# Optimization experiments

Hardware: AMD Instinct MI355X
Metric: run time of the kernel (lower is better)

## Reference

```python
import jax, jax.numpy as jnp
import numpy as np

WS = 8   # window_size
SS = 4   # shift_size
NH = 6   # num_heads
EPS = 1e-5


def _win_partition(x, ws):
    # x: [B, H, W, C] -> [B * H/ws * W/ws, ws*ws, C]
    B, H, W, C = x.shape
    x = x.reshape(B, H // ws, ws, W // ws, ws, C)
    return x.transpose(0, 1, 3, 2, 4, 5).reshape(-1, ws * ws, C)


def _win_reverse(wins, ws, H, W, B):
    C = wins.shape[-1]
    x = wins.reshape(B, H // ws, W // ws, ws, ws, C)
    return x.transpose(0, 1, 3, 2, 4, 5).reshape(B, H, W, C)


def _rel_pos_index(ws):
    # static numpy computation, identical to the torch buffer
    coords = np.stack(np.meshgrid(np.arange(ws), np.arange(ws), indexing='ij')).reshape(2, -1)
    rel = coords[:, :, None] - coords[:, None, :]          # [2, N, N]
    rel = rel.transpose(1, 2, 0).copy()                    # [N, N, 2]
    rel[..., 0] += ws - 1
    rel[..., 1] += ws - 1
    rel[..., 0] *= 2 * ws - 1
    return rel.sum(-1)                                     # [N, N] int


def _attn_mask_np(H, W, ws, ss):
    # static numpy computation of the SW-MSA mask, identical to _compute_mask
    img = np.zeros((1, H, W, 1), np.float32)
    cnt = 0
    for hs in (slice(0, -ws), slice(-ws, -ss), slice(-ss, None)):
        for wsl in (slice(0, -ws), slice(-ws, -ss), slice(-ss, None)):
            img[:, hs, wsl, :] = cnt
            cnt += 1
    mw = img.reshape(1, H // ws, ws, W // ws, ws, 1).transpose(0, 1, 3, 2, 4, 5).reshape(-1, ws * ws)
    am = mw[:, None, :] - mw[:, :, None]                   # [nW, N, N]
    return np.where(am != 0, np.float32(-100.0), np.float32(0.0))


def _swin_forward(x, qkv_w, qkv_b, proj_w, proj_b, rpb_table,
                  norm2_g, norm2_b, mlp_w1, mlp_b1, mlp_w2, mlp_b2, H, W):
    B, L, C = x.shape
    ws, ss, nh = WS, SS, NH
    hd = C // nh
    x2d = x.reshape(B, H, W, C)
    shifted = jnp.roll(x2d, (-ss, -ss), axis=(1, 2))
    win = _win_partition(shifted, ws)                      # [B_, N, C]
    B_, N, _ = win.shape

    # --- window attention (note: original applies attention to un-normalized x) ---
    qkv = (win @ qkv_w + qkv_b).reshape(B_, N, 3, nh, hd)
    q = qkv[:, :, 0].transpose(0, 2, 1, 3)                 # [B_, nh, N, hd]
    k = qkv[:, :, 1].transpose(0, 2, 1, 3)
    v = qkv[:, :, 2].transpose(0, 2, 1, 3)
    attn = jnp.einsum('bhnd,bhmd->bhnm', q, k) * (hd ** -0.5)

    bias = rpb_table[jnp.asarray(_rel_pos_index(ws)).reshape(-1)]
    bias = bias.reshape(N, N, nh).transpose(2, 0, 1)       # [nh, N, N]
    attn = attn + bias[None]

    mask = jnp.asarray(_attn_mask_np(H, W, ws, ss))        # [nW, N, N]
    nW = mask.shape[0]
    attn = attn.reshape(B_ // nW, nW, nh, N, N) + mask[None, :, None]
    attn = jax.nn.softmax(attn.reshape(B_, nh, N, N), axis=-1)

    out = jnp.einsum('bhnm,bhmd->bnhd', attn, v).reshape(B_, N, C)
    out = out @ proj_w + proj_b

    x2d = _win_reverse(out, ws, H, W, B)
    x2d = jnp.roll(x2d, (ss, ss), axis=(1, 2))
    x = x + x2d.reshape(B, L, C)

    # --- MLP branch with LayerNorm (norm2) ---
    mu = x.mean(-1, keepdims=True)
    var = x.var(-1, keepdims=True)
    xn = (x - mu) * jax.lax.rsqrt(var + EPS) * norm2_g + norm2_b
    h = jax.nn.gelu(xn @ mlp_w1 + mlp_b1, approximate=False)
    return x + (h @ mlp_w2 + mlp_b2)


def setup_inputs() -> dict:
    B, H, W, C = 8, 128, 128, 192
    mlp_hidden = 4 * C
    ks = jax.random.split(jax.random.key(0), 6)
    std = 0.02
    return {
        'x': jax.random.normal(ks[0], (B, H * W, C), jnp.float32),
        'qkv_w': jax.random.normal(ks[1], (C, 3 * C), jnp.float32) * std,
        'qkv_b': jnp.zeros((3 * C,), jnp.float32),
        'proj_w': jax.random.normal(ks[2], (C, C), jnp.float32) * std,
        'proj_b': jnp.zeros((C,), jnp.float32),
        'rpb_table': jax.random.normal(ks[3], ((2 * WS - 1) ** 2, NH), jnp.float32) * std,
        'norm2_g': jnp.ones((C,), jnp.float32),
        'norm2_b': jnp.zeros((C,), jnp.float32),
        'mlp_w1': jax.random.normal(ks[4], (C, mlp_hidden), jnp.float32) * std,
        'mlp_b1': jnp.zeros((mlp_hidden,), jnp.float32),
        'mlp_w2': jax.random.normal(ks[5], (mlp_hidden, C), jnp.float32) * std,
        'mlp_b2': jnp.zeros((C,), jnp.float32),
        'H': H,
        'W': W,
    }


def reference(x, qkv_w, qkv_b, proj_w, proj_b, rpb_table, norm2_g, norm2_b,
              mlp_w1, mlp_b1, mlp_w2, mlp_b2, H, W):
    return _swin_forward(x, qkv_w, qkv_b, proj_w, proj_b, rpb_table,
                         norm2_g, norm2_b, mlp_w1, mlp_b1, mlp_w2, mlp_b2, H, W)
```

## Files before the change

kernel.cpp:

```cpp
#include <hip/hip_runtime.h>
#include <hip/hip_bf16.h>


typedef __hip_bfloat16 bf16;
typedef __attribute__((ext_vector_type(8))) short bfrag;
typedef __attribute__((ext_vector_type(4))) float ffrag;

union bfu { bf16 h[8]; bfrag v; };

__device__ __forceinline__ float b2f(bf16 v) { return __bfloat162float(v); }
__device__ __forceinline__ bf16  f2b(float v) { return __float2bfloat16(v); }

#define MFMA(a, b, c) __builtin_amdgcn_mfma_f32_16x16x32_bf16((a), (b), (c), 0, 0, 0)

#define WS_XRES  0ULL
#define WS_OG    100663296ULL
#define WS_QKVTG 150994944ULL
#define WS_QBG   151250944ULL
#define WS_PROJT 151253504ULL
#define WS_W1T   151330304ULL
#define WS_W2T   151637504ULL
#define WS_SB    151969280ULL

__device__ __forceinline__ void stage_lds(const void* g, void* l, int nbytes, int t) {
    const int lane16 = (t & 63) * 16;
    for (int base = (t >> 6) * 1024; base < nbytes; base += 4096) {
        if (base + lane16 < nbytes) {
            __builtin_amdgcn_global_load_lds(
                (const __attribute__((address_space(1))) void*)((const char*)g + base + lane16),
                (__attribute__((address_space(3))) void*)((char*)l + base),
                16, 0, 0);
        }
    }
}

__device__ __forceinline__ float gelu_t(float x) {
    float y = x * (1.5957691216057308f + 0.07135481627f * x * x);
    return x * (1.f / (1.f + __expf(-y)));
}

__global__ __launch_bounds__(256) void k_prep(
    const float* __restrict__ qkv_w, const float* __restrict__ qkv_b,
    const float* __restrict__ proj_w, const float* __restrict__ w1,
    const float* __restrict__ w2, const float* __restrict__ rpb,
    char* __restrict__ ws)
{
    int i = blockIdx.x * 256 + threadIdx.x;
    bf16*  qkvTg = (bf16*)(ws + WS_QKVTG);
    float* qbg   = (float*)(ws + WS_QBG);
    bf16*  projT = (bf16*)(ws + WS_PROJT);
    bf16*  w1T   = (bf16*)(ws + WS_W1T);
    bf16*  w2T   = (bf16*)(ws + WS_W2T);
    bf16*  sbB   = (bf16*)(ws + WS_SB);

    if (i < 128000) {
        int g = i / 64000, rem = i % 64000;
        int c = rem / 200, k = rem % 200;
        float v = 0.f;
        if (k < 192 && c < 288) {
            int h = g * 3 + c / 96, j = c % 96;
            int src = (j < 32) ? (h * 32 + j)
                    : (j < 64) ? (192 + h * 32 + (j - 32))
                               : (384 + h * 32 + (j - 64));
            v = qkv_w[k * 576 + src];
        }
        qkvTg[i] = f2b(v);
    } else if (i < 128640) {
        int j = i - 128000;
        int g = j / 320, c = j % 320;
        float v = 0.f;
        if (c < 288) {
            int h = g * 3 + c / 96, jj = c % 96;
            int src = (jj < 32) ? (h * 32 + jj)
                    : (jj < 64) ? (192 + h * 32 + (jj - 32))
                                : (384 + h * 32 + (jj - 64));
            v = qkv_b[src];
        }
        qbg[j] = v;
    } else if (i < 167040) {
        int j = i - 128640;
        int c = j / 200, k = j % 200;
        projT[j] = f2b(k < 192 ? proj_w[k * 192 + c] : 0.f);
    } else if (i < 320640) {
        int j = i - 167040;
        int c = j / 200, k = j % 200;
        w1T[j] = f2b(k < 192 ? w1[k * 768 + c] : 0.f);
    } else if (i < 486528) {
        int j = i - 320640;
        int kc = j / 13824, r = (j % 13824) / 72, kk = j % 72;
        w2T[j] = f2b(kk < 64 ? w2[(kc * 64 + kk) * 192 + r] : 0.f);
    } else if (i < 584832) {
        int j = i - 486528;
        int cls = j / 24576, h = (j % 24576) / 4096;
        int ii = (j % 4096) / 64, jj = j % 64;
        int ri = ii >> 3, ci = ii & 7, rj = jj >> 3, cj = jj & 7;
        float bias = rpb[(((ri - rj + 7) * 15) + (ci - cj + 7)) * 6 + h];
        int clsR = cls >> 1, clsC = cls & 1;
        int regi = (clsR ? (ri < 4 ? 1 : 2) : 0) * 3 + (clsC ? (ci < 4 ? 1 : 2) : 0);
        int regj = (clsR ? (rj < 4 ? 1 : 2) : 0) * 3 + (clsC ? (cj < 4 ? 1 : 2) : 0);
        sbB[j] = f2b(bias + (regi == regj ? 0.f : -100.f));
    }
}

__global__ __launch_bounds__(256, 3) void k_attn(
    const float* __restrict__ x, const char* __restrict__ ws,
    bf16* __restrict__ Og)
{
    __shared__ __align__(16) unsigned char smem[52224];
    bf16*  sWb = (bf16*)(smem);
    bf16*  sQh = (bf16*)(smem + 25600);
    bf16*  sKh = (bf16*)(smem + 30720);
    bf16*  sVT = (bf16*)(smem + 35840);
    bf16*  sP  = (bf16*)(smem + 40448);
    float* sQB = (float*)(smem + 49664);

    const bf16*  qkvTg = (const bf16*)(ws + WS_QKVTG);
    const float* qbg   = (const float*)(ws + WS_QBG);
    const bf16*  sbB   = (const bf16*)(ws + WS_SB);

    const int t    = threadIdx.x;
    const int lane = t & 63, quad = lane >> 4, l15 = lane & 15;
    const int wave = t >> 6, r0 = wave * 16;
    const int win = blockIdx.x;
    const int b   = win >> 8;
    const int wi  = win & 255;
    const int wh  = wi >> 4, wwi = wi & 15;

    stage_lds(qbg, smem + 49664, 2560, t);
    stage_lds(qkvTg, sWb, 12800, t);

    bfrag aX[6];
    {
        int row = r0 + l15;
        int rr = row >> 3, cc = row & 7;
        int hs  = (wh * 8 + rr + 4) & 127;
        int wsx = (wwi * 8 + cc + 4) & 127;
        const float* xrow = x + ((size_t)(b * 16384 + hs * 128 + wsx)) * 192;
        #pragma unroll
        for (int kb = 0; kb < 6; kb++) {
            float4 f0 = *(const float4*)(xrow + kb * 32 + quad * 8);
            float4 f1 = *(const float4*)(xrow + kb * 32 + quad * 8 + 4);
            bfu u;
            u.h[0] = f2b(f0.x); u.h[1] = f2b(f0.y); u.h[2] = f2b(f0.z); u.h[3] = f2b(f0.w);
            u.h[4] = f2b(f1.x); u.h[5] = f2b(f1.y); u.h[6] = f2b(f1.z); u.h[7] = f2b(f1.w);
            aX[kb] = u.v;
        }
    }

    const int cls = ((wh == 15) ? 2 : 0) + ((wwi == 15) ? 1 : 0);
    const bf16* bBc = sbB + (size_t)cls * 24576;
    bf16* sPw = sP + wave * 16 * 72;

    __syncthreads();

    int pb = 0;
    int cb = 0;
    for (int cc = 0; cc < 18; cc++) {
        const int h = cc / 3, cpart = cc - h * 3;
        if (cc < 17) {
            int cbn = (cc == 8) ? 320 : cb + 32;
            stage_lds(qkvTg + (size_t)cbn * 200, sWb + (pb ^ 1) * 6400, 12800, t);
        }
        const bf16* sW = sWb + pb * 6400;
        #pragma unroll
        for (int ct = 0; ct < 2; ct++) {
            bfrag bw[6];
            #pragma unroll
            for (int kb = 0; kb < 6; kb++)
                bw[kb] = *(const bfrag*)&sW[(ct * 16 + l15) * 200 + kb * 32 + quad * 8];
            ffrag acc = {0.f, 0.f, 0.f, 0.f};
            #pragma unroll
            for (int kb = 0; kb < 6; kb++) acc = MFMA(aX[kb], bw[kb], acc);
            float bias = sQB[cb + ct * 16 + l15];
            const int cl = ct * 16 + l15;
            #pragma unroll
            for (int reg = 0; reg < 4; reg++) {
                int r = r0 + quad * 4 + reg;
                float v = acc[reg] + bias;
                if (cpart == 0)      sQh[r * 40 + cl] = f2b(v);
                else if (cpart == 1) sKh[r * 40 + cl] = f2b(v);
                else                 sVT[cl * 72 + r] = f2b(v);
            }
        }
        __syncthreads();
        pb ^= 1;
        cb = (cc == 8) ? 320 : cb + 32;

        if (cpart == 2) {
            bfrag aQ = *(const bfrag*)&sQh[(r0 + l15) * 40 + quad * 8];
            ffrag Sf[4];
            #pragma unroll
            for (int jt = 0; jt < 4; jt++) {
                bfrag bK = *(const bfrag*)&sKh[(jt * 16 + l15) * 40 + quad * 8];
                ffrag z = {0.f, 0.f, 0.f, 0.f};
                Sf[jt] = MFMA(aQ, bK, z);
            }
            const bf16* bb = bBc + h * 4096 + (r0 + quad * 4) * 64 + l15;
            #pragma unroll
            for (int jt = 0; jt < 4; jt++)
                #pragma unroll
                for (int reg = 0; reg < 4; reg++)
                    Sf[jt][reg] = Sf[jt][reg] * 0.1767766952966369f
                                + b2f(bb[reg * 64 + jt * 16]);
            #pragma unroll
            for (int reg = 0; reg < 4; reg++) {
                float m = fmaxf(fmaxf(Sf[0][reg], Sf[1][reg]), fmaxf(Sf[2][reg], Sf[3][reg]));
                m = fmaxf(m, __shfl_xor(m, 1)); m = fmaxf(m, __shfl_xor(m, 2));
                m = fmaxf(m, __shfl_xor(m, 4)); m = fmaxf(m, __shfl_xor(m, 8));
                float s = 0.f;
                #pragma unroll
                for (int jt = 0; jt < 4; jt++) { Sf[jt][reg] = __expf(Sf[jt][reg] - m); s += Sf[jt][reg]; }
                s += __shfl_xor(s, 1); s += __shfl_xor(s, 2);
                s += __shfl_xor(s, 4); s += __shfl_xor(s, 8);
                float inv = 1.f / s;
                int prow = (quad * 4 + reg) * 72;
                #pragma unroll
                for (int jt = 0; jt < 4; jt++)
                    sPw[prow + jt * 16 + l15] = f2b(Sf[jt][reg] * inv);
            }
            bfrag aP0 = *(const bfrag*)&sPw[l15 * 72 + quad * 8];
            bfrag aP1 = *(const bfrag*)&sPw[l15 * 72 + 32 + quad * 8];
            #pragma unroll
            for (int ct = 0; ct < 2; ct++) {
                bfrag bV0 = *(const bfrag*)&sVT[(ct * 16 + l15) * 72 + quad * 8];
                bfrag bV1 = *(const bfrag*)&sVT[(ct * 16 + l15) * 72 + 32 + quad * 8];
                ffrag z = {0.f, 0.f, 0.f, 0.f};
                ffrag o = MFMA(aP1, bV1, MFMA(aP0, bV0, z));
                #pragma unroll
                for (int reg = 0; reg < 4; reg++)
                    Og[((size_t)win * 64 + r0 + quad * 4 + reg) * 192 + h * 32 + ct * 16 + l15]
                        = f2b(o[reg]);
            }
            if (cc < 17) __syncthreads();
        }
    }
}

__global__ __launch_bounds__(256, 2) void k_proj(
    const float* __restrict__ x, const float* __restrict__ proj_b,
    const char* __restrict__ ws, float* __restrict__ xres)
{
    __shared__ __align__(16) bf16 sWp[192 * 200];

    const bf16* projT = (const bf16*)(ws + WS_PROJT);
    const bf16* Og    = (const bf16*)(ws + WS_OG);

    const int t    = threadIdx.x;
    const int lane = t & 63, quad = lane >> 4, l15 = lane & 15;
    const int wave = t >> 6, r0 = wave * 32;
    const size_t row0 = (size_t)blockIdx.x * 128;

    stage_lds(projT, sWp, 76800, t);

    bfrag aO[2][6];
    #pragma unroll
    for (int rt = 0; rt < 2; rt++)
        #pragma unroll
        for (int kb = 0; kb < 6; kb++)
            aO[rt][kb] = *(const bfrag*)&Og[(row0 + r0 + rt * 16 + l15) * 192 + kb * 32 + quad * 8];

    size_t tokb[2][4];
    #pragma unroll
    for (int rt = 0; rt < 2; rt++)
        #pragma unroll
        for (int reg = 0; reg < 4; reg++) {
            int n = r0 + rt * 16 + quad * 4 + reg;
            int w2 = (int)(blockIdx.x * 2) + (n >> 6);
            int nl = n & 63;
            int b = w2 >> 8, wi = w2 & 255;
            int wh = wi >> 4, wwi = wi & 15;
            int sr = wh * 8 + (nl >> 3), sc = wwi * 8 + (nl & 7);
            int h2 = (sr + 4) & 127, w2c = (sc + 4) & 127;
            tokb[rt][reg] = ((size_t)(b * 16384 + h2 * 128 + w2c)) * 192;
        }

    __syncthreads();

    ffrag acc[2][12];
    #pragma unroll
    for (int rt = 0; rt < 2; rt++)
        #pragma unroll
        for (int ct = 0; ct < 12; ct++)
            acc[rt][ct] = (ffrag){0.f, 0.f, 0.f, 0.f};

    #pragma unroll
    for (int ct = 0; ct < 12; ct++) {
        bfrag bw[6];
        #pragma unroll
        for (int kb = 0; kb < 6; kb++)
            bw[kb] = *(const bfrag*)&sWp[(ct * 16 + l15) * 200 + kb * 32 + quad * 8];
        #pragma unroll
        for (int rt = 0; rt < 2; rt++)
            #pragma unroll
            for (int kb = 0; kb < 6; kb++)
                acc[rt][ct] = MFMA(aO[rt][kb], bw[kb], acc[rt][ct]);
    }

    #pragma unroll
    for (int rt = 0; rt < 2; rt++)
        #pragma unroll
        for (int ct = 0; ct < 12; ct++) {
            int col = ct * 16 + l15;
            float pb = proj_b[col];
            #pragma unroll
            for (int reg = 0; reg < 4; reg++) {
                size_t gi = tokb[rt][reg] + col;
                xres[gi] = acc[rt][ct][reg] + pb + x[gi];
            }
        }
}

__global__ __launch_bounds__(256, 2) void k_mlp(
    const float* __restrict__ xres, const float* __restrict__ g,
    const float* __restrict__ bb, const float* __restrict__ b1,
    const float* __restrict__ b2, const char* __restrict__ ws,
    float* __restrict__ out)
{
    __shared__ __align__(16) unsigned char smem[71680];
    bf16* U   = (bf16*)(smem);
    bf16* W2s = (bf16*)(smem + 25600);
    bf16* hS  = (bf16*)(smem + 53248);

    const bf16* w1T = (const bf16*)(ws + WS_W1T);
    const bf16* w2T = (const bf16*)(ws + WS_W2T);

    const int t    = threadIdx.x;
    const int lane = t & 63, quad = lane >> 4, l15 = lane & 15;
    const int wave = t >> 6, r0 = wave * 32;
    const size_t row0 = (size_t)blockIdx.x * 128;

    #pragma unroll
    for (int p = 0; p < 2; p++) {
        int row = r0 + p * 16 + l15;
        const float4* src = (const float4*)(xres + (row0 + row) * 192 + quad * 48);
        float v[48];
        float s = 0.f, sq = 0.f;
        #pragma unroll
        for (int u = 0; u < 12; u++) {
            float4 f = src[u];
            v[u*4] = f.x; v[u*4+1] = f.y; v[u*4+2] = f.z; v[u*4+3] = f.w;
            s  += f.x + f.y + f.z + f.w;
            sq += f.x*f.x + f.y*f.y + f.z*f.z + f.w*f.w;
        }
        s  += __shfl_xor(s, 16);  s  += __shfl_xor(s, 32);
        sq += __shfl_xor(sq, 16); sq += __shfl_xor(sq, 32);
        float mean = s * (1.f / 192.f);
        float var  = sq * (1.f / 192.f) - mean * mean;
        float rstd = rsqrtf(var + 1e-5f);
        __hip_bfloat162* dst = (__hip_bfloat162*)&U[row * 200 + quad * 48];
        #pragma unroll
        for (int u = 0; u < 24; u++) {
            int c = quad * 48 + u * 2;
            float a0 = (v[u*2]   - mean) * rstd * g[c]     + bb[c];
            float a1 = (v[u*2+1] - mean) * rstd * g[c + 1] + bb[c + 1];
            dst[u] = __float22bfloat162_rn({a0, a1});
        }
    }

    bfrag aX[2][6];
    #pragma unroll
    for (int rt = 0; rt < 2; rt++)
        #pragma unroll
        for (int kb = 0; kb < 6; kb++)
            aX[rt][kb] = *(const bfrag*)&U[(r0 + rt*16 + l15) * 200 + kb*32 + quad*8];

    __syncthreads();

    bf16* hs_w = hS + wave * 32 * 72;

    ffrag oacc[2][12];
    #pragma unroll
    for (int rt = 0; rt < 2; rt++)
        #pragma unroll
        for (int ct = 0; ct < 12; ct++)
            oacc[rt][ct] = (ffrag){0.f, 0.f, 0.f, 0.f};

    for (int kc = 0; kc < 12; kc++) {
        __syncthreads();
        stage_lds(w1T + (size_t)kc * 64 * 200, U, 25600, t);
        stage_lds(w2T + (size_t)kc * 13824, W2s, 27648, t);
        __syncthreads();

        #pragma unroll
        for (int ct = 0; ct < 4; ct++) {
            bfrag bw[6];
            #pragma unroll
            for (int kb = 0; kb < 6; kb++)
                bw[kb] = *(const bfrag*)&U[(ct*16 + l15) * 200 + kb*32 + quad*8];
            float bias = b1[kc * 64 + ct * 16 + l15];
            #pragma unroll
            for (int rt = 0; rt < 2; rt++) {
                ffrag a = {0.f, 0.f, 0.f, 0.f};
                #pragma unroll
                for (int kb = 0; kb < 6; kb++) a = MFMA(aX[rt][kb], bw[kb], a);
                #pragma unroll
                for (int reg = 0; reg < 4; reg++)
                    hs_w[(rt*16 + quad*4 + reg) * 72 + ct*16 + l15] =
                        f2b(gelu_t(a[reg] + bias));
            }
        }
        bfrag aH[2][2];
        #pragma unroll
        for (int rt = 0; rt < 2; rt++)
            #pragma unroll
            for (int k0 = 0; k0 < 2; k0++)
                aH[rt][k0] = *(const bfrag*)&hs_w[(rt*16 + l15) * 72 + k0*32 + quad*8];
        #pragma unroll
        for (int ct = 0; ct < 12; ct++) {
            bfrag bw2[2];
            #pragma unroll
            for (int k0 = 0; k0 < 2; k0++)
                bw2[k0] = *(const bfrag*)&W2s[(ct*16 + l15) * 72 + k0*32 + quad*8];
            #pragma unroll
            for (int rt = 0; rt < 2; rt++)
                #pragma unroll
                for (int k0 = 0; k0 < 2; k0++)
                    oacc[rt][ct] = MFMA(aH[rt][k0], bw2[k0], oacc[rt][ct]);
        }
    }

    #pragma unroll
    for (int rt = 0; rt < 2; rt++)
        #pragma unroll
        for (int ct = 0; ct < 12; ct++) {
            int col = ct * 16 + l15;
            float b2v = b2[col];
            #pragma unroll
            for (int reg = 0; reg < 4; reg++) {
                size_t gi = (row0 + r0 + rt*16 + quad*4 + reg) * 192 + col;
                out[gi] = xres[gi] + oacc[rt][ct][reg] + b2v;
            }
        }
}

extern "C" void kernel_launch(void* const* d_in, const int* in_sizes, int n_in,
                              void* d_out, int out_size, void* d_ws, size_t ws_size,
                              hipStream_t stream)
{
    (void)in_sizes; (void)n_in; (void)out_size; (void)ws_size;

    const float* x      = (const float*)d_in[0];
    const float* qkv_w  = (const float*)d_in[1];
    const float* qkv_b  = (const float*)d_in[2];
    const float* proj_w = (const float*)d_in[3];
    const float* proj_b = (const float*)d_in[4];
    const float* rpb    = (const float*)d_in[5];
    const float* n2g    = (const float*)d_in[6];
    const float* n2b    = (const float*)d_in[7];
    const float* w1     = (const float*)d_in[8];
    const float* b1     = (const float*)d_in[9];
    const float* w2     = (const float*)d_in[10];
    const float* b2     = (const float*)d_in[11];

    char*  ws   = (char*)d_ws;
    float* xres = (float*)(ws + WS_XRES);
    bf16*  Og   = (bf16*)(ws + WS_OG);
    float* out  = (float*)d_out;

    hipLaunchKernelGGL(k_prep, dim3(2285), dim3(256), 0, stream,
                       qkv_w, qkv_b, proj_w, w1, w2, rpb, ws);
    hipLaunchKernelGGL(k_attn, dim3(2048), dim3(256), 0, stream,
                       x, ws, Og);
    hipLaunchKernelGGL(k_proj, dim3(1024), dim3(256), 0, stream,
                       x, proj_b, ws, xres);
    hipLaunchKernelGGL(k_mlp,  dim3(1024), dim3(256), 0, stream,
                       xres, n2g, n2b, b1, b2, ws, out);
}
```

Baseline: 479.0 us.

## Fuse output projection and residual into attention kernel per head

```diff
diff --git a/kernel.cpp b/kernel.cpp
--- a/kernel.cpp
+++ b/kernel.cpp
@@ -21,6 +21,7 @@
 #define WS_W1T   151330304ULL
 #define WS_W2T   151637504ULL
 #define WS_SB    151969280ULL
+#define WS_PROJH 152165888ULL
 
 __device__ __forceinline__ void stage_lds(const void* g, void* l, int nbytes, int t) {
     const int lane16 = (t & 63) * 16;
@@ -52,6 +53,7 @@
     bf16*  w1T   = (bf16*)(ws + WS_W1T);
     bf16*  w2T   = (bf16*)(ws + WS_W2T);
     bf16*  sbB   = (bf16*)(ws + WS_SB);
+    bf16*  projH = (bf16*)(ws + WS_PROJH);
 
     if (i < 128000) {
         int g = i / 64000, rem = i % 64000;
@@ -99,24 +101,30 @@
         int regi = (clsR ? (ri < 4 ? 1 : 2) : 0) * 3 + (clsC ? (ci < 4 ? 1 : 2) : 0);
         int regj = (clsR ? (rj < 4 ? 1 : 2) : 0) * 3 + (clsC ? (cj < 4 ? 1 : 2) : 0);
         sbB[j] = f2b(bias + (regi == regj ? 0.f : -100.f));
-    }
-}
-
-__global__ __launch_bounds__(256, 3) void k_attn(
+    } else if (i < 630912) {
+        int j = i - 584832;
+        int s = j / 7680, c = (j % 7680) / 40, kk = j % 40;
+        projH[j] = f2b(kk < 32 ? proj_w[(s * 32 + kk) * 192 + c] : 0.f);
+    }
+}
+
+__global__ __launch_bounds__(256, 2) void k_attn(
     const float* __restrict__ x, const char* __restrict__ ws,
-    bf16* __restrict__ Og)
+    const float* __restrict__ proj_b, float* __restrict__ xres)
 {
-    __shared__ __align__(16) unsigned char smem[52224];
-    bf16*  sWb = (bf16*)(smem);
-    bf16*  sQh = (bf16*)(smem + 25600);
-    bf16*  sKh = (bf16*)(smem + 30720);
-    bf16*  sVT = (bf16*)(smem + 35840);
-    bf16*  sP  = (bf16*)(smem + 40448);
-    float* sQB = (float*)(smem + 49664);
+    __shared__ __align__(16) unsigned char smem[67584];
+    bf16*  sWb   = (bf16*)(smem);
+    bf16*  sQh   = (bf16*)(smem + 25600);
+    bf16*  sKh   = (bf16*)(smem + 30720);
+    bf16*  sVT   = (bf16*)(smem + 35840);
+    bf16*  sP    = (bf16*)(smem + 40448);
+    float* sQB   = (float*)(smem + 49664);
+    bf16*  sProj = (bf16*)(smem + 52224);
 
     const bf16*  qkvTg = (const bf16*)(ws + WS_QKVTG);
     const float* qbg   = (const float*)(ws + WS_QBG);
     const bf16*  sbB   = (const bf16*)(ws + WS_SB);
+    const bf16*  projH = (const bf16*)(ws + WS_PROJH);
 
     const int t    = threadIdx.x;
     const int lane = t & 63, quad = lane >> 4, l15 = lane & 15;
@@ -128,6 +136,7 @@
 
     stage_lds(qbg, smem + 49664, 2560, t);
     stage_lds(qkvTg, sWb, 12800, t);
+    stage_lds(projH, sProj, 15360, t);
 
     bfrag aX[6];
     {
@@ -147,9 +156,23 @@
         }
     }
 
+    size_t tokb[4];
+    #pragma unroll
+    for (int reg = 0; reg < 4; reg++) {
+        int nl = r0 + quad * 4 + reg;
+        int sr = wh * 8 + (nl >> 3), sc = wwi * 8 + (nl & 7);
+        int h2 = (sr + 4) & 127, w2c = (sc + 4) & 127;
+        tokb[reg] = ((size_t)(b * 16384 + h2 * 128 + w2c)) * 192;
+    }
+
     const int cls = ((wh == 15) ? 2 : 0) + ((wwi == 15) ? 1 : 0);
     const bf16* bBc = sbB + (size_t)cls * 24576;
     bf16* sPw = sP + wave * 16 * 72;
+
+    ffrag acc[12];
+    #pragma unroll
+    for (int ct = 0; ct < 12; ct++)
+        acc[ct] = (ffrag){0.f, 0.f, 0.f, 0.f};
 
     __syncthreads();
 
@@ -161,6 +184,9 @@
             int cbn = (cc == 8) ? 320 : cb + 32;
             stage_lds(qkvTg + (size_t)cbn * 200, sWb + (pb ^ 1) * 6400, 12800, t);
         }
+        if (cpart == 1 && cc >= 4)
+            stage_lds(projH + (size_t)h * 7680, sProj, 15360, t);
+
         const bf16* sW = sWb + pb * 6400;
         #pragma unroll
         for (int ct = 0; ct < 2; ct++) {
@@ -168,15 +194,15 @@
             #pragma unroll
             for (int kb = 0; kb < 6; kb++)
                 bw[kb] = *(const bfrag*)&sW[(ct * 16 + l15) * 200 + kb * 32 + quad * 8];
-            ffrag acc = {0.f, 0.f, 0.f, 0.f};
-            #pragma unroll
-            for (int kb = 0; kb < 6; kb++) acc = MFMA(aX[kb], bw[kb], acc);
+            ffrag qacc = {0.f, 0.f, 0.f, 0.f};
+            #pragma unroll
+            for (int kb = 0; kb < 6; kb++) qacc = MFMA(aX[kb], bw[kb], qacc);
             float bias = sQB[cb + ct * 16 + l15];
             const int cl = ct * 16 + l15;
             #pragma unroll
             for (int reg = 0; reg < 4; reg++) {
                 int r = r0 + quad * 4 + reg;
-                float v = acc[reg] + bias;
+                float v = qacc[reg] + bias;
                 if (cpart == 0)      sQh[r * 40 + cl] = f2b(v);
                 else if (cpart == 1) sKh[r * 40 + cl] = f2b(v);
                 else                 sVT[cl * 72 + r] = f2b(v);
@@ -220,94 +246,39 @@
             }
             bfrag aP0 = *(const bfrag*)&sPw[l15 * 72 + quad * 8];
             bfrag aP1 = *(const bfrag*)&sPw[l15 * 72 + 32 + quad * 8];
+            ffrag o[2];
             #pragma unroll
             for (int ct = 0; ct < 2; ct++) {
                 bfrag bV0 = *(const bfrag*)&sVT[(ct * 16 + l15) * 72 + quad * 8];
                 bfrag bV1 = *(const bfrag*)&sVT[(ct * 16 + l15) * 72 + 32 + quad * 8];
                 ffrag z = {0.f, 0.f, 0.f, 0.f};
-                ffrag o = MFMA(aP1, bV1, MFMA(aP0, bV0, z));
+                o[ct] = MFMA(aP1, bV1, MFMA(aP0, bV0, z));
+            }
+            #pragma unroll
+            for (int ct = 0; ct < 2; ct++)
                 #pragma unroll
                 for (int reg = 0; reg < 4; reg++)
-                    Og[((size_t)win * 64 + r0 + quad * 4 + reg) * 192 + h * 32 + ct * 16 + l15]
-                        = f2b(o[reg]);
+                    sPw[(quad * 4 + reg) * 40 + ct * 16 + l15] = f2b(o[ct][reg]);
+            bfrag aO = *(const bfrag*)&sPw[l15 * 40 + quad * 8];
+            #pragma unroll
+            for (int ct2 = 0; ct2 < 12; ct2++) {
+                bfrag bwp = *(const bfrag*)&sProj[(ct2 * 16 + l15) * 40 + quad * 8];
+                acc[ct2] = MFMA(aO, bwp, acc[ct2]);
             }
             if (cc < 17) __syncthreads();
         }
     }
-}
-
-__global__ __launch_bounds__(256, 2) void k_proj(
-    const float* __restrict__ x, const float* __restrict__ proj_b,
-    const char* __restrict__ ws, float* __restrict__ xres)
-{
-    __shared__ __align__(16) bf16 sWp[192 * 200];
-
-    const bf16* projT = (const bf16*)(ws + WS_PROJT);
-    const bf16* Og    = (const bf16*)(ws + WS_OG);
-
-    const int t    = threadIdx.x;
-    const int lane = t & 63, quad = lane >> 4, l15 = lane & 15;
-    const int wave = t >> 6, r0 = wave * 32;
-    const size_t row0 = (size_t)blockIdx.x * 128;
-
-    stage_lds(projT, sWp, 76800, t);
-
-    bfrag aO[2][6];
-    #pragma unroll
-    for (int rt = 0; rt < 2; rt++)
-        #pragma unroll
-        for (int kb = 0; kb < 6; kb++)
-            aO[rt][kb] = *(const bfrag*)&Og[(row0 + r0 + rt * 16 + l15) * 192 + kb * 32 + quad * 8];
-
-    size_t tokb[2][4];
-    #pragma unroll
-    for (int rt = 0; rt < 2; rt++)
+
+    #pragma unroll
+    for (int ct2 = 0; ct2 < 12; ct2++) {
+        int col = ct2 * 16 + l15;
+        float pbv = proj_b[col];
         #pragma unroll
         for (int reg = 0; reg < 4; reg++) {
-            int n = r0 + rt * 16 + quad * 4 + reg;
-            int w2 = (int)(blockIdx.x * 2) + (n >> 6);
-            int nl = n & 63;
-            int b = w2 >> 8, wi = w2 & 255;
-            int wh = wi >> 4, wwi = wi & 15;
-            int sr = wh * 8 + (nl >> 3), sc = wwi * 8 + (nl & 7);
-            int h2 = (sr + 4) & 127, w2c = (sc + 4) & 127;
-            tokb[rt][reg] = ((size_t)(b * 16384 + h2 * 128 + w2c)) * 192;
-        }
-
-    __syncthreads();
-
-    ffrag acc[2][12];
-    #pragma unroll
-    for (int rt = 0; rt < 2; rt++)
-        #pragma unroll
-        for (int ct = 0; ct < 12; ct++)
-            acc[rt][ct] = (ffrag){0.f, 0.f, 0.f, 0.f};
-
-    #pragma unroll
-    for (int ct = 0; ct < 12; ct++) {
-        bfrag bw[6];
-        #pragma unroll
-        for (int kb = 0; kb < 6; kb++)
-            bw[kb] = *(const bfrag*)&sWp[(ct * 16 + l15) * 200 + kb * 32 + quad * 8];
-        #pragma unroll
-        for (int rt = 0; rt < 2; rt++)
-            #pragma unroll
-            for (int kb = 0; kb < 6; kb++)
-                acc[rt][ct] = MFMA(aO[rt][kb], bw[kb], acc[rt][ct]);
-    }
-
-    #pragma unroll
-    for (int rt = 0; rt < 2; rt++)
-        #pragma unroll
-        for (int ct = 0; ct < 12; ct++) {
-            int col = ct * 16 + l15;
-            float pb = proj_b[col];
-            #pragma unroll
-            for (int reg = 0; reg < 4; reg++) {
-                size_t gi = tokb[rt][reg] + col;
-                xres[gi] = acc[rt][ct][reg] + pb + x[gi];
-            }
-        }
+            size_t gi = tokb[reg] + col;
+            xres[gi] = acc[ct2][reg] + pbv + x[gi];
+        }
+    }
 }
 
 __global__ __launch_bounds__(256, 2) void k_mlp(
@@ -454,15 +425,12 @@
 
     char*  ws   = (char*)d_ws;
     float* xres = (float*)(ws + WS_XRES);
-    bf16*  Og   = (bf16*)(ws + WS_OG);
     float* out  = (float*)d_out;
 
-    hipLaunchKernelGGL(k_prep, dim3(2285), dim3(256), 0, stream,
+    hipLaunchKernelGGL(k_prep, dim3(2465), dim3(256), 0, stream,
                        qkv_w, qkv_b, proj_w, w1, w2, rpb, ws);
     hipLaunchKernelGGL(k_attn, dim3(2048), dim3(256), 0, stream,
-                       x, ws, Og);
-    hipLaunchKernelGGL(k_proj, dim3(1024), dim3(256), 0, stream,
-                       x, proj_b, ws, xres);
+                       x, ws, proj_b, xres);
     hipLaunchKernelGGL(k_mlp,  dim3(1024), dim3(256), 0, stream,
                        xres, n2g, n2b, b1, b2, ws, out);
 }
```

After: 470.5 us. Within noise of the previous version (-1.8%).
